# Kernel optimization log

Measured on AMD Instinct MI355X. Metric: run time of the kernel, lower is better.

Reference implementation:

```python
import jax, jax.numpy as jnp
import numpy as np

# Model hyperparameters (match init_kwargs params)
HIDDEN = 512
ALPHA = 1.0 / 10.0                      # dt / tau
G = 1.5
SIGMA_REC = G / np.sqrt(HIDDEN)
ADD_NOISE = 1.0
NOISE_SCALE = np.sqrt(2.0 * SIGMA_REC ** 2 / ALPHA) * ADD_NOISE


def setup_inputs() -> dict:
    key = jax.random.key(0)
    ks = jax.random.split(key, 11)
    T, B, I, H, O, OC = 2048, 64, 64, HIDDEN, 32, 8
    return {
        "input_sig": jax.random.normal(ks[0], (T, B, I), dtype=jnp.float32),
        "rate0": jax.random.uniform(ks[1], (B, H), dtype=jnp.float32, minval=-1.0, maxval=1.0),
        "noise": jax.random.normal(ks[2], (T, B, H), dtype=jnp.float32),
        "Wi": jax.random.normal(ks[3], (H, I), dtype=jnp.float32) * SIGMA_REC,
        "bi": jax.random.normal(ks[4], (H,), dtype=jnp.float32) * 0.01,
        "Wh": jax.random.normal(ks[5], (H, H), dtype=jnp.float32) * SIGMA_REC,
        "bh": jax.random.normal(ks[6], (H,), dtype=jnp.float32) * 0.01,
        "Wo": jax.random.normal(ks[7], (O, H), dtype=jnp.float32) * SIGMA_REC,
        "bo": jax.random.normal(ks[8], (O,), dtype=jnp.float32) * 0.01,
        "Woc": jax.random.normal(ks[9], (OC, H), dtype=jnp.float32),
        "boc": jax.random.normal(ks[10], (OC,), dtype=jnp.float32) * 0.01,
    }


def reference(input_sig, rate0, noise, Wi, bi, Wh, bh, Wo, bo, Woc, boc):
    # forward_dual: leaky-integration chaotic RNN over time, then two readouts.
    alpha = jnp.float32(ALPHA)
    nscale = jnp.float32(NOISE_SCALE)

    def step(rate, xs):
        x_t, n_t = xs  # [B,I], [B,H]
        pre = x_t @ Wi.T + bi + rate @ Wh.T + bh + n_t * nscale
        rate_new = (1.0 - alpha) * rate + alpha * jnp.tanh(pre)
        return rate_new, rate_new

    _, rate_all = jax.lax.scan(step, rate0, (input_sig, noise))  # [T,B,H]
    output = jnp.einsum('tbh,oh->tbo', rate_all, Wo) + bo          # [T,B,O]
    output_ctx = jnp.einsum('tbh,ch->tbc', rate_all, Woc) + boc    # [T,B,OC]
    return (output, output_ctx, rate_all)
```

## Files before the change

### kernel.cpp

```cpp
#include <hip/hip_runtime.h>
#include <math.h>

#define TT 2048
#define BB 64
#define II 64
#define HH 512
#define OO 32
#define OCC 8
#define QS 128
#define WT_LD 48

#define OUT1_OFF ((size_t)TT * BB * OO)
#define RATE_OFF (OUT1_OFF + (size_t)TT * BB * OCC)

#define FLAG_BYTE_OFF ((size_t)1 << 20)
#define FLAG_BYTES (BB * 4 * 16 * sizeof(int))
#define WT_BYTE_OFF ((size_t)2 << 20)

__global__ __launch_bounds__(256) void pack_wt(
    const float* __restrict__ Wo, const float* __restrict__ Woc,
    float* __restrict__ Wt)
{
    int idx = blockIdx.x * 256 + threadIdx.x;
    if (idx >= HH * WT_LD) return;
    int h = idx / WT_LD, o = idx % WT_LD;
    float v = 0.f;
    if (o < OO)            v = Wo[(size_t)o * HH + h];
    else if (o < OO + OCC) v = Woc[(size_t)(o - OO) * HH + h];
    Wt[idx] = v;
}

__global__ __launch_bounds__(1024) void rnn_scan12(
    const float* __restrict__ x,
    const float* __restrict__ rate0,
    const float* __restrict__ noise,
    const float* __restrict__ Wh,
    const float* __restrict__ Wi,
    const float* __restrict__ bi,
    const float* __restrict__ bh,
    float* __restrict__ rate_out,
    float* P,
    int* flags)
{
    __shared__ float  st[QS];
    __shared__ float  parts[8 * HH];
    __shared__ float4 wi4[II / 4][QS];
    __shared__ float4 xbuf4[II / 4];

    const int bid = blockIdx.x;
    const int q   = bid >> 6;
    const int b   = bid & 63;
    const int tid = threadIdx.x;
    const int g   = tid >> 7;
    const int ht  = tid & 127;
    const int h4  = 4 * ht;
    const int kq  = q * QS + g * 16;

    const double SIG = 1.5 / sqrt(512.0);
    const float  NS  = (float)sqrt(2.0 * SIG * SIG / 0.1);

    float4 wreg[16];
    #pragma unroll
    for (int m = 0; m < 16; ++m) {
        wreg[m].x = Wh[(size_t)(h4 + 0) * HH + kq + m];
        wreg[m].y = Wh[(size_t)(h4 + 1) * HH + kq + m];
        wreg[m].z = Wh[(size_t)(h4 + 2) * HH + kq + m];
        wreg[m].w = Wh[(size_t)(h4 + 3) * HH + kq + m];
    }

    for (int i = tid; i < QS * (II / 4); i += 1024) {
        int l = i >> 4, c4 = i & 15;
        wi4[c4][l] = *(const float4*)&Wi[(size_t)(q * QS + l) * II + 4 * c4];
    }

    const bool inband = (tid >= q * QS) && (tid < q * QS + QS);
    const int  l      = tid - q * QS;
    float rf = 0.f, bsum = 0.f;
    if (inband) {
        rf   = rate0[b * HH + tid];
        bsum = bi[tid] + bh[tid];
    }
    if (tid < QS) st[tid] = rate0[b * HH + q * QS + tid];
    int* myflag = &flags[(b * 4 + q) * 16];
    __syncthreads();

    for (int t = 0; t < TT; ++t) {
        const int par = t & 1;
        const size_t row = ((size_t)t * BB + b) * HH;

        if (tid < II / 4)
            xbuf4[tid] = *(const float4*)&x[((size_t)t * BB + b) * II + 4 * tid];
        float nz = 0.f;
        if (inband) nz = noise[row + tid];

        float a0 = 0.f, a1 = 0.f, a2 = 0.f, a3 = 0.f;
        #pragma unroll
        for (int mm = 0; mm < 4; ++mm) {
            float4 s4 = *(const float4*)&st[g * 16 + 4 * mm];
            a0 += wreg[4*mm].x*s4.x + wreg[4*mm+1].x*s4.y + wreg[4*mm+2].x*s4.z + wreg[4*mm+3].x*s4.w;
            a1 += wreg[4*mm].y*s4.x + wreg[4*mm+1].y*s4.y + wreg[4*mm+2].y*s4.z + wreg[4*mm+3].y*s4.w;
            a2 += wreg[4*mm].z*s4.x + wreg[4*mm+1].z*s4.y + wreg[4*mm+2].z*s4.z + wreg[4*mm+3].z*s4.w;
            a3 += wreg[4*mm].w*s4.x + wreg[4*mm+1].w*s4.y + wreg[4*mm+2].w*s4.z + wreg[4*mm+3].w*s4.w;
        }
        *(float4*)&parts[g * HH + h4] = make_float4(a0, a1, a2, a3);
        __syncthreads();

        float s = 0.f;
        if (tid < HH) {
            #pragma unroll
            for (int p = 0; p < 8; ++p) s += parts[p * HH + tid];
            if (!inband)
                __hip_atomic_store(&P[(((size_t)b * 4 + q) * 2 + par) * HH + tid], s,
                                   __ATOMIC_RELAXED, __HIP_MEMORY_SCOPE_AGENT);
        }
        __syncthreads();

        if (tid == 0)
            __hip_atomic_store(myflag, t + 1, __ATOMIC_RELAXED,
                               __HIP_MEMORY_SCOPE_AGENT);

        float pre = 0.f;
        if (inband) {
            pre = bsum + NS * nz;
            #pragma unroll
            for (int c4 = 0; c4 < II / 4; ++c4) {
                float4 wv = wi4[c4][l];
                float4 xv = xbuf4[c4];
                pre += wv.x * xv.x + wv.y * xv.y + wv.z * xv.z + wv.w * xv.w;
            }
        }

        if (tid == 64 || tid == 128 || tid == 192) {
            int* f = &flags[(b * 4 + ((q + (tid >> 6)) & 3)) * 16];
            while (__hip_atomic_load(f, __ATOMIC_RELAXED,
                                     __HIP_MEMORY_SCOPE_AGENT) < t + 1) {}
        }
        __syncthreads();

        if (inband) {
            float tot = pre + s;
            #pragma unroll
            for (int j = 1; j < 4; ++j) {
                const int pj = (q + j) & 3;
                tot += __hip_atomic_load(
                    &P[(((size_t)b * 4 + pj) * 2 + par) * HH + tid],
                    __ATOMIC_RELAXED, __HIP_MEMORY_SCOPE_AGENT);
            }
            rf = 0.9f * rf + 0.1f * tanhf(tot);
            rate_out[row + tid] = rf;
            st[l] = rf;
        }
        __syncthreads();
    }
}

__global__ __launch_bounds__(512) void readout2(
    const float* __restrict__ rate_all,
    const float* __restrict__ Wt,
    const float* __restrict__ bo, const float* __restrict__ boc,
    float* __restrict__ out, float* __restrict__ outc)
{
    __shared__ float rbuf[16][HH];
    const int tid  = threadIdx.x;
    const size_t row0 = (size_t)blockIdx.x * 16;

    for (int i = tid; i < 16 * (HH / 4); i += 512) {
        int r = i >> 7, c = (i & 127) * 4;
        *(float4*)&rbuf[r][c] = *(const float4*)&rate_all[(row0 + r) * HH + c];
    }
    __syncthreads();

    {
        const int r = tid >> 5, o = tid & 31;
        const float* wt = Wt + o;
        float acc = 0.f;
        #pragma unroll 8
        for (int h = 0; h < HH; h += 4) {
            float4 rv = *(const float4*)&rbuf[r][h];
            acc += rv.x * wt[(size_t)(h + 0) * WT_LD]
                 + rv.y * wt[(size_t)(h + 1) * WT_LD]
                 + rv.z * wt[(size_t)(h + 2) * WT_LD]
                 + rv.w * wt[(size_t)(h + 3) * WT_LD];
        }
        out[(row0 + r) * OO + o] = acc + bo[o];
    }
    if (tid < 128) {
        const int r = tid >> 3, c = tid & 7;
        const float* wt = Wt + OO + c;
        float acc = 0.f;
        #pragma unroll 8
        for (int h = 0; h < HH; h += 4) {
            float4 rv = *(const float4*)&rbuf[r][h];
            acc += rv.x * wt[(size_t)(h + 0) * WT_LD]
                 + rv.y * wt[(size_t)(h + 1) * WT_LD]
                 + rv.z * wt[(size_t)(h + 2) * WT_LD]
                 + rv.w * wt[(size_t)(h + 3) * WT_LD];
        }
        outc[(row0 + r) * OCC + c] = acc + boc[c];
    }
}

extern "C" void kernel_launch(void* const* d_in, const int* in_sizes, int n_in,
                              void* d_out, int out_size, void* d_ws, size_t ws_size,
                              hipStream_t stream)
{
    const float* x     = (const float*)d_in[0];
    const float* rate0 = (const float*)d_in[1];
    const float* noise = (const float*)d_in[2];
    const float* Wi    = (const float*)d_in[3];
    const float* bi    = (const float*)d_in[4];
    const float* Wh    = (const float*)d_in[5];
    const float* bh    = (const float*)d_in[6];
    const float* Wo    = (const float*)d_in[7];
    const float* bo    = (const float*)d_in[8];
    const float* Woc   = (const float*)d_in[9];
    const float* boc   = (const float*)d_in[10];

    float* out   = (float*)d_out;
    float* rateb = out + RATE_OFF;
    float* P     = (float*)d_ws;
    int*   flags = (int*)((char*)d_ws + FLAG_BYTE_OFF);
    float* Wt    = (float*)((char*)d_ws + WT_BYTE_OFF);

    hipMemsetAsync(flags, 0, FLAG_BYTES, stream);
    pack_wt<<<(HH * WT_LD + 255) / 256, 256, 0, stream>>>(Wo, Woc, Wt);
    rnn_scan12<<<4 * BB, 1024, 0, stream>>>(x, rate0, noise, Wh, Wi, bi, bh,
                                            rateb, P, flags);
    readout2<<<TT * BB / 16, 512, 0, stream>>>(rateb, Wt, bo, boc,
                                               out, out + OUT1_OFF);
}
```

Before: 4.837 ms.

## Restructure cross-block exchange with per-destination flags and wave-specialized producers

Each of the four blocks that share a batch row now publishes its partial sums per destination slice, packing two floats into one 64-bit relaxed store. A dedicated wave signals a per-slot flag for each destination, and separate waves spin on the incoming flags, so one intra-block barrier drops out of every timestep. The input projection and noise load now overlap with the publish and wait work. This relies on s_waitcnt ordering with relaxed atomics for correctness, and the spin waits still add latency on each step.

```diff
diff --git a/kernel.cpp b/kernel.cpp
--- a/kernel.cpp
+++ b/kernel.cpp
@@ -13,8 +13,10 @@
 #define OUT1_OFF ((size_t)TT * BB * OO)
 #define RATE_OFF (OUT1_OFF + (size_t)TT * BB * OCC)
 
-#define FLAG_BYTE_OFF ((size_t)1 << 20)
-#define FLAG_BYTES (BB * 4 * 16 * sizeof(int))
+#define P2_IDX(b,p,slot,par) ((((((size_t)(b) * 4 + (p)) * 3 + (slot)) * 2 + (par)) * 64))
+#define FLAG_BYTE_OFF ((size_t)0x180000)
+#define FLAG_IDX(b,p,slot) ((((b) * 4 + (p)) * 3 + (slot)) * 16)
+#define FLAG_BYTES (BB * 4 * 3 * 16 * sizeof(int))
 #define WT_BYTE_OFF ((size_t)2 << 20)
 
 __global__ __launch_bounds__(256) void pack_wt(
@@ -30,7 +32,7 @@
     Wt[idx] = v;
 }
 
-__global__ __launch_bounds__(1024) void rnn_scan12(
+__global__ __launch_bounds__(1024) void rnn_scan13(
     const float* __restrict__ x,
     const float* __restrict__ rate0,
     const float* __restrict__ noise,
@@ -39,7 +41,7 @@
     const float* __restrict__ bi,
     const float* __restrict__ bh,
     float* __restrict__ rate_out,
-    float* P,
+    unsigned long long* P2,
     int* flags)
 {
     __shared__ float  st[QS];
@@ -55,6 +57,8 @@
     const int ht  = tid & 127;
     const int h4  = 4 * ht;
     const int kq  = q * QS + g * 16;
+    const int wv  = tid >> 6;
+    const int lane = tid & 63;
 
     const double SIG = 1.5 / sqrt(512.0);
     const float  NS  = (float)sqrt(2.0 * SIG * SIG / 0.1);
@@ -69,8 +73,8 @@
     }
 
     for (int i = tid; i < QS * (II / 4); i += 1024) {
-        int l = i >> 4, c4 = i & 15;
-        wi4[c4][l] = *(const float4*)&Wi[(size_t)(q * QS + l) * II + 4 * c4];
+        int l2 = i >> 4, c4 = i & 15;
+        wi4[c4][l2] = *(const float4*)&Wi[(size_t)(q * QS + l2) * II + 4 * c4];
     }
 
     const bool inband = (tid >= q * QS) && (tid < q * QS + QS);
@@ -81,7 +85,6 @@
         bsum = bi[tid] + bh[tid];
     }
     if (tid < QS) st[tid] = rate0[b * HH + q * QS + tid];
-    int* myflag = &flags[(b * 4 + q) * 16];
     __syncthreads();
 
     for (int t = 0; t < TT; ++t) {
@@ -90,8 +93,6 @@
 
         if (tid < II / 4)
             xbuf4[tid] = *(const float4*)&x[((size_t)t * BB + b) * II + 4 * tid];
-        float nz = 0.f;
-        if (inband) nz = noise[row + tid];
 
         float a0 = 0.f, a1 = 0.f, a2 = 0.f, a3 = 0.f;
         #pragma unroll
@@ -105,35 +106,44 @@
         *(float4*)&parts[g * HH + h4] = make_float4(a0, a1, a2, a3);
         __syncthreads();
 
-        float s = 0.f;
-        if (tid < HH) {
+        float s = 0.f, pre = 0.f;
+        if (inband) {
+            float nz = noise[row + tid];
             #pragma unroll
             for (int p = 0; p < 8; ++p) s += parts[p * HH + tid];
-            if (!inband)
-                __hip_atomic_store(&P[(((size_t)b * 4 + q) * 2 + par) * HH + tid], s,
+            pre = bsum + NS * nz;
+            #pragma unroll
+            for (int c4 = 0; c4 < II / 4; ++c4) {
+                float4 wv4 = wi4[c4][l];
+                float4 xv  = xbuf4[c4];
+                pre += wv4.x * xv.x + wv4.y * xv.y + wv4.z * xv.z + wv4.w * xv.w;
+            }
+        } else if (wv >= 8 && wv < 11) {
+            const int j  = wv - 7;
+            const int pj = (q + j) & 3;
+            const int hb = pj * QS + lane;
+            float slo = 0.f, shi = 0.f;
+            #pragma unroll
+            for (int p = 0; p < 8; ++p) {
+                slo += parts[p * HH + hb];
+                shi += parts[p * HH + hb + 64];
+            }
+            unsigned long long w =
+                ((unsigned long long)__float_as_uint(shi) << 32) | __float_as_uint(slo);
+            __hip_atomic_store(&P2[P2_IDX(b, q, j - 1, par) + lane], w,
+                               __ATOMIC_RELAXED, __HIP_MEMORY_SCOPE_AGENT);
+            asm volatile("s_waitcnt vmcnt(0)" ::: "memory");
+            if (lane == 0)
+                __hip_atomic_store(&flags[FLAG_IDX(b, q, j - 1)], t + 1,
                                    __ATOMIC_RELAXED, __HIP_MEMORY_SCOPE_AGENT);
-        }
-        __syncthreads();
-
-        if (tid == 0)
-            __hip_atomic_store(myflag, t + 1, __ATOMIC_RELAXED,
-                               __HIP_MEMORY_SCOPE_AGENT);
-
-        float pre = 0.f;
-        if (inband) {
-            pre = bsum + NS * nz;
-            #pragma unroll
-            for (int c4 = 0; c4 < II / 4; ++c4) {
-                float4 wv = wi4[c4][l];
-                float4 xv = xbuf4[c4];
-                pre += wv.x * xv.x + wv.y * xv.y + wv.z * xv.z + wv.w * xv.w;
-            }
-        }
-
-        if (tid == 64 || tid == 128 || tid == 192) {
-            int* f = &flags[(b * 4 + ((q + (tid >> 6)) & 3)) * 16];
-            while (__hip_atomic_load(f, __ATOMIC_RELAXED,
-                                     __HIP_MEMORY_SCOPE_AGENT) < t + 1) {}
+        } else if (wv >= 11 && wv < 14) {
+            if (lane == 0) {
+                const int j  = wv - 10;
+                const int pj = (q + j) & 3;
+                int* f = &flags[FLAG_IDX(b, pj, 3 - j)];
+                while (__hip_atomic_load(f, __ATOMIC_RELAXED,
+                                         __HIP_MEMORY_SCOPE_AGENT) < t + 1) {}
+            }
         }
         __syncthreads();
 
@@ -142,9 +152,11 @@
             #pragma unroll
             for (int j = 1; j < 4; ++j) {
                 const int pj = (q + j) & 3;
-                tot += __hip_atomic_load(
-                    &P[(((size_t)b * 4 + pj) * 2 + par) * HH + tid],
+                unsigned long long u = __hip_atomic_load(
+                    &P2[P2_IDX(b, pj, 3 - j, par) + (l & 63)],
                     __ATOMIC_RELAXED, __HIP_MEMORY_SCOPE_AGENT);
+                unsigned bits = (l >> 6) ? (unsigned)(u >> 32) : (unsigned)u;
+                tot += __uint_as_float(bits);
             }
             rf = 0.9f * rf + 0.1f * tanhf(tot);
             rate_out[row + tid] = rf;
@@ -218,14 +230,14 @@
 
     float* out   = (float*)d_out;
     float* rateb = out + RATE_OFF;
-    float* P     = (float*)d_ws;
+    unsigned long long* P2 = (unsigned long long*)d_ws;
     int*   flags = (int*)((char*)d_ws + FLAG_BYTE_OFF);
     float* Wt    = (float*)((char*)d_ws + WT_BYTE_OFF);
 
     hipMemsetAsync(flags, 0, FLAG_BYTES, stream);
     pack_wt<<<(HH * WT_LD + 255) / 256, 256, 0, stream>>>(Wo, Woc, Wt);
-    rnn_scan12<<<4 * BB, 1024, 0, stream>>>(x, rate0, noise, Wh, Wi, bi, bh,
-                                            rateb, P, flags);
+    rnn_scan13<<<4 * BB, 1024, 0, stream>>>(x, rate0, noise, Wh, Wi, bi, bh,
+                                            rateb, P2, flags);
     readout2<<<TT * BB / 16, 512, 0, stream>>>(rateb, Wt, bo, boc,
                                                out, out + OUT1_OFF);
 }
```

Result: slower. 8.368 ms (+73.0%).
